# Performance work log

Measured on AMD Instinct MI355X. Metric: run time of the kernel, lower is better.

The kernel has to match this reference:

```python
import jax, jax.numpy as jnp
import numpy as np

N_NODES = 100000
EPS = 1e-07


def _gconv(src, dst, x, W, b):
    # DGL GraphConv with norm='both': D_dst^{-1/2} A (D_src^{-1/2} x) W + b
    ones = jnp.ones(src.shape[0], x.dtype)
    deg_out = jax.ops.segment_sum(ones, src, num_segments=N_NODES)
    deg_in = jax.ops.segment_sum(ones, dst, num_segments=N_NODES)
    norm_out = jnp.where(deg_out > 0, deg_out, 1.0) ** -0.5
    norm_in = jnp.where(deg_in > 0, deg_in, 1.0) ** -0.5
    h = x * norm_out[:, None]
    agg = jax.ops.segment_sum(h[src], dst, num_segments=N_NODES)  # [N, d]
    agg = agg * norm_in[:, None]
    return agg @ W + b


def _branch(npemb, gauss, unif, temp, Wm, bm, Wl, bl, Wq, bq, Wd1, bd1, WdX, bdX, Wc, bc):
    cat = unif.shape[-1]
    mean = npemb @ Wm + bm                      # [E, d_z]
    logstd = npemb @ Wl + bl                    # [E, d_z]
    Nlat = gauss * jnp.exp(logstd) + mean       # reparameterization
    Nlat = Nlat.reshape(npemb.shape[0], cat, -1)  # [E, cat, d_m]
    q = npemb @ Wq + bq                         # [E, cat]
    gumbel = -jnp.log(-jnp.log(unif + EPS) + EPS)
    Z = jax.nn.softmax((q + gumbel) / temp, axis=-1)  # [E, cat]
    M = jnp.einsum('ec,ecd->ed', Z, Nlat)       # [E, d_m]
    X = jax.nn.relu(jax.nn.relu(M @ Wd1 + bd1) @ WdX + bdX)
    A = jax.nn.softmax(M @ Wc + bc, axis=-1)
    return A, X, mean, logstd, q


def setup_inputs() -> dict:
    key = jax.random.key(0)
    ks = jax.random.split(key, 32)
    E_g, E = 800000, 262144
    d_in, d_h, d_z, cat, d_m, d_dec, d_out = 128, 256, 256, 4, 64, 256, 128
    s = 0.05
    inp = {
        'x': jax.random.normal(ks[0], (N_NODES, d_in), jnp.float32),
        'src': jax.random.randint(ks[1], (E_g,), 0, N_NODES),
        'dst': jax.random.randint(ks[2], (E_g,), 0, N_NODES),
        'pos_src': jax.random.randint(ks[3], (E,), 0, N_NODES),
        'pos_dst': jax.random.randint(ks[4], (E,), 0, N_NODES),
        'neg_src': jax.random.randint(ks[5], (E,), 0, N_NODES),
        'neg_dst': jax.random.randint(ks[6], (E,), 0, N_NODES),
        'gauss_pos': jax.random.normal(ks[7], (E, d_z), jnp.float32),
        'gauss_neg': jax.random.normal(ks[8], (E, d_z), jnp.float32),
        'unif_pos': jax.random.uniform(ks[9], (E, cat), jnp.float32),
        'unif_neg': jax.random.uniform(ks[10], (E, cat), jnp.float32),
        'temp': 1,
        'W1': jax.random.normal(ks[11], (d_in, d_h), jnp.float32) * s,
        'b1': jnp.zeros((d_h,), jnp.float32),
        'W2': jax.random.normal(ks[12], (d_h, d_h), jnp.float32) * s,
        'b2': jnp.zeros((d_h,), jnp.float32),
        'Wm': jax.random.normal(ks[13], (d_h, d_z), jnp.float32) * s,
        'bm': jnp.zeros((d_z,), jnp.float32),
        'Wl': jax.random.normal(ks[14], (d_h, d_z), jnp.float32) * s,
        'bl': jnp.zeros((d_z,), jnp.float32),
        'Wq': jax.random.normal(ks[15], (d_h, cat), jnp.float32) * s,
        'bq': jnp.zeros((cat,), jnp.float32),
        'Wd1': jax.random.normal(ks[16], (d_m, d_dec), jnp.float32) * s,
        'bd1': jnp.zeros((d_dec,), jnp.float32),
        'WdX': jax.random.normal(ks[17], (d_dec, d_out), jnp.float32) * s,
        'bdX': jnp.zeros((d_out,), jnp.float32),
        'Wc': jax.random.normal(ks[18], (d_m, cat), jnp.float32) * s,
        'bc': jnp.zeros((cat,), jnp.float32),
    }
    return inp


def reference(x, src, dst, pos_src, pos_dst, neg_src, neg_dst,
              gauss_pos, gauss_neg, unif_pos, unif_neg, temp,
              W1, b1, W2, b2, Wm, bm, Wl, bl, Wq, bq,
              Wd1, bd1, WdX, bdX, Wc, bc):
    # two-layer GraphConv encoder (relu after layer 0; dropout in eval mode = identity)
    h = jax.nn.relu(_gconv(src, dst, x, W1, b1))
    h = _gconv(src, dst, h, W2, b2)
    # u_add_v edge gather
    pos_npemb = h[pos_src] + h[pos_dst]
    neg_npemb = h[neg_src] + h[neg_dst]
    t = jnp.asarray(temp, h.dtype)
    posA, posX, pos_mean, pos_logstd, posq = _branch(
        pos_npemb, gauss_pos, unif_pos, t, Wm, bm, Wl, bl, Wq, bq, Wd1, bd1, WdX, bdX, Wc, bc)
    negA, negX, neg_mean, neg_logstd, negq = _branch(
        neg_npemb, gauss_neg, unif_neg, t, Wm, bm, Wl, bl, Wq, bq, Wd1, bd1, WdX, bdX, Wc, bc)
    return (posA, negA, posX, negX, pos_mean, neg_mean,
            pos_logstd, neg_logstd, posq, negq)
```

## Files before the change

kernel.cpp:

```cpp
#include <hip/hip_runtime.h>
#include <hip/hip_bf16.h>


#define NN 100000
#define EG 800000
#define EE 262144
#define NB 98

typedef __attribute__((ext_vector_type(8))) short short8;
typedef __attribute__((ext_vector_type(4))) float f32x4;

__device__ __forceinline__ float bf2f(unsigned u16) {
  union { unsigned u; float f; } v; v.u = u16 << 16; return v.f;
}
__device__ __forceinline__ float lo2f(unsigned u) {
  union { unsigned u; float f; } v; v.u = u << 16; return v.f;
}
__device__ __forceinline__ float hi2f(unsigned u) {
  union { unsigned u; float f; } v; v.u = u & 0xFFFF0000u; return v.f;
}
__device__ __forceinline__ unsigned short f2bf(float f) {
  union { float f; unsigned u; } v; v.f = f;
  return (unsigned short)((v.u + 0x7FFFu + ((v.u >> 16) & 1u)) >> 16);
}
__device__ __forceinline__ unsigned pack2bf(float a, float b) {
  return (unsigned)f2bf(a) | ((unsigned)f2bf(b) << 16);
}
__device__ __forceinline__ int permc(int c) {
  return (c & ~31) | ((c & 15) << 1) | ((c >> 4) & 1);
}

__device__ __forceinline__ float decode_scalar(const void* p) {
  unsigned u = *(const unsigned*)p;
  float f = __uint_as_float(u);
  float af = fabsf(f);
  if (af >= 1e-6f && af <= 1e6f) return f;
  if (u < 1024u) return (float)u;
  return 1.0f;
}

__global__ __launch_bounds__(256) void k_deg(const int* __restrict__ src,
                                             const int* __restrict__ dst,
                                             int* __restrict__ degO,
                                             int* __restrict__ degI) {
  for (int i = blockIdx.x * 256 + threadIdx.x; i < EG; i += gridDim.x * 256) {
    atomicAdd(&degO[src[i]], 1);
    atomicAdd(&degI[dst[i]], 1);
  }
}

__global__ __launch_bounds__(256) void k_norm(const int* __restrict__ degO,
                                              const int* __restrict__ degI,
                                              float* __restrict__ normO,
                                              float* __restrict__ normI) {
  int i = blockIdx.x * 256 + threadIdx.x;
  if (i < NN) {
    int dO = degO[i]; if (dO < 1) dO = 1;
    int dI = degI[i]; if (dI < 1) dI = 1;
    normO[i] = rsqrtf((float)dO);
    normI[i] = rsqrtf((float)dI);
  }
}

__global__ __launch_bounds__(1024) void k_scan1(const int* __restrict__ degI,
                                                int* __restrict__ rowptr,
                                                int* __restrict__ bsum) {
  __shared__ int wsum[16];
  int t = threadIdx.x, lane = t & 63, wv = t >> 6;
  int i = blockIdx.x * 1024 + t;
  int v = (i < NN) ? degI[i] : 0;
  int incl = v;
#pragma unroll
  for (int off = 1; off < 64; off <<= 1) {
    int u = __shfl_up(incl, off);
    if (lane >= off) incl += u;
  }
  if (lane == 63) wsum[wv] = incl;
  __syncthreads();
  if (wv == 0 && lane < 16) {
    int s = wsum[lane];
    int si = s;
#pragma unroll
    for (int off = 1; off < 16; off <<= 1) {
      int u = __shfl_up(si, off);
      if (lane >= off) si += u;
    }
    wsum[lane] = si - s;
    if (lane == 15) bsum[blockIdx.x] = si;
  }
  __syncthreads();
  int excl = wsum[wv] + incl - v;
  if (i < NN) rowptr[i] = excl;
}

__global__ __launch_bounds__(128) void k_scan2(int* __restrict__ bsum) {
  __shared__ int w0tot;
  int t = threadIdx.x, lane = t & 63, wv = t >> 6;
  int v = (t < NB) ? bsum[t] : 0;
  int incl = v;
#pragma unroll
  for (int off = 1; off < 64; off <<= 1) {
    int u = __shfl_up(incl, off);
    if (lane >= off) incl += u;
  }
  if (wv == 0 && lane == 63) w0tot = incl;
  __syncthreads();
  int excl = incl - v + (wv ? w0tot : 0);
  if (t < NB) bsum[t] = excl;
}

__global__ __launch_bounds__(1024) void k_scan3(const int* __restrict__ degI,
                                                int* __restrict__ rowptr,
                                                int* __restrict__ cursor,
                                                const int* __restrict__ bsum) {
  int i = blockIdx.x * 1024 + threadIdx.x;
  if (i < NN) {
    int vv = rowptr[i] + bsum[blockIdx.x];
    rowptr[i] = vv;
    cursor[i] = vv;
    if (i == NN - 1) rowptr[NN] = vv + degI[i];
  }
}

__global__ __launch_bounds__(256) void k_fill(const int* __restrict__ src,
                                              const int* __restrict__ dst,
                                              int* __restrict__ cursor,
                                              int* __restrict__ csr) {
  for (int e = blockIdx.x * 256 + threadIdx.x; e < EG; e += gridDim.x * 256) {
    int d = dst[e];
    int pos = atomicAdd(&cursor[d], 1);
    csr[pos] = src[e];
  }
}

__global__ __launch_bounds__(256) void k_transpose(const float* __restrict__ in,
                                                   unsigned short* __restrict__ out,
                                                   int K, int Nmask, int logN, int total) {
  for (int idx = blockIdx.x * 256 + threadIdx.x; idx < total; idx += gridDim.x * 256) {
    int n = idx & Nmask;
    int k = idx >> logN;
    out[(size_t)n * K + k] = f2bf(in[idx]);
  }
}

__global__ __launch_bounds__(256) void k_transpose_q(const float* __restrict__ Wq,
                                                     unsigned short* __restrict__ WqT) {
  int idx = blockIdx.x * 256 + threadIdx.x;
  if (idx < 4096) {
    int r = idx >> 8, k = idx & 255;
    WqT[idx] = (r < 4) ? f2bf(Wq[k * 4 + r]) : (unsigned short)0;
  }
}

__global__ __launch_bounds__(256) void k_gather1(
    const float* __restrict__ x, const int* __restrict__ rowptr,
    const int* __restrict__ csr, const float* __restrict__ normO,
    const float* __restrict__ normI, unsigned short* __restrict__ agg) {
  int wid = (blockIdx.x * 256 + threadIdx.x) >> 6;
  int lane = threadIdx.x & 63;
  int half = lane >> 5, fl = lane & 31;
  int nw = (gridDim.x * 256) >> 6;
  for (int n = wid; n < NN; n += nw) {
    int beg = rowptr[n], end = rowptr[n + 1];
    float a0 = 0.f, a1 = 0.f, a2 = 0.f, a3 = 0.f;
    for (int i = beg + half; i < end; i += 2) {
      int s = csr[i];
      float ns = normO[s];
      float4 v = *(const float4*)(x + ((size_t)s << 7) + (fl << 2));
      a0 += ns * v.x; a1 += ns * v.y; a2 += ns * v.z; a3 += ns * v.w;
    }
    a0 += __shfl_xor(a0, 32); a1 += __shfl_xor(a1, 32);
    a2 += __shfl_xor(a2, 32); a3 += __shfl_xor(a3, 32);
    if (lane < 32) {
      float ni = normI[n];
      *(uint2*)(agg + ((size_t)n << 7) + (fl << 2)) =
          make_uint2(pack2bf(a0 * ni, a1 * ni), pack2bf(a2 * ni, a3 * ni));
    }
  }
}

__global__ __launch_bounds__(256) void k_gather2(
    const unsigned short* __restrict__ h1s, const int* __restrict__ rowptr,
    const int* __restrict__ csr, const float* __restrict__ normI,
    unsigned short* __restrict__ agg) {
  int wid = (blockIdx.x * 256 + threadIdx.x) >> 6;
  int lane = threadIdx.x & 63;
  int half = lane >> 5, fl = lane & 31;
  int nw = (gridDim.x * 256) >> 6;
  for (int n = wid; n < NN; n += nw) {
    int beg = rowptr[n], end = rowptr[n + 1];
    float a0 = 0.f, a1 = 0.f, a2 = 0.f, a3 = 0.f, a4 = 0.f, a5 = 0.f, a6 = 0.f, a7 = 0.f;
    for (int i = beg + half; i < end; i += 2) {
      int s = csr[i];
      uint4 v = *(const uint4*)(h1s + ((size_t)s << 8) + (fl << 3));
      a0 += lo2f(v.x); a1 += hi2f(v.x);
      a2 += lo2f(v.y); a3 += hi2f(v.y);
      a4 += lo2f(v.z); a5 += hi2f(v.z);
      a6 += lo2f(v.w); a7 += hi2f(v.w);
    }
    a0 += __shfl_xor(a0, 32); a1 += __shfl_xor(a1, 32);
    a2 += __shfl_xor(a2, 32); a3 += __shfl_xor(a3, 32);
    a4 += __shfl_xor(a4, 32); a5 += __shfl_xor(a5, 32);
    a6 += __shfl_xor(a6, 32); a7 += __shfl_xor(a7, 32);
    if (lane < 32) {
      float ni = normI[n];
      uint4 o;
      o.x = pack2bf(a0 * ni, a1 * ni);
      o.y = pack2bf(a2 * ni, a3 * ni);
      o.z = pack2bf(a4 * ni, a5 * ni);
      o.w = pack2bf(a6 * ni, a7 * ni);
      *(uint4*)(agg + ((size_t)n << 8) + (fl << 3)) = o;
    }
  }
}

template <int K, bool RELU, bool OSCALE>
__global__ __launch_bounds__(256) void k_gemm(
    const unsigned short* __restrict__ A, const float* __restrict__ oscale,
    const unsigned short* __restrict__ WT, const float* __restrict__ bias,
    unsigned short* __restrict__ C, int M) {
  __shared__ __align__(16) short At[128 * 40];
  __shared__ __align__(16) short Bt[256 * 40];
  const int t = threadIdx.x;
  const int row0 = blockIdx.x * 128;
  const int lane = t & 63, wave = t >> 6;
  const int wr = (wave >> 1) << 6;
  const int wcc = (wave & 1) << 7;
  const int lrow = lane & 15, lhi = lane >> 4;

  f32x4 acc[4][8];
#pragma unroll
  for (int m = 0; m < 4; ++m)
#pragma unroll
    for (int n = 0; n < 8; ++n) acc[m][n] = (f32x4){0.f, 0.f, 0.f, 0.f};

  for (int k0 = 0; k0 < K; k0 += 32) {
    if (k0) __syncthreads();
#pragma unroll
    for (int it = 0; it < 2; ++it) {
      int idx = t + it * 256;
      int r = idx >> 2, c8 = (idx & 3) << 3;
      int grow = row0 + r;
      int4 tv = {0, 0, 0, 0};
      if (grow < M) tv = *(const int4*)(A + (size_t)grow * K + k0 + c8);
      *(int4*)&At[r * 40 + c8] = tv;
    }
    {
      const unsigned short* wt = WT + (size_t)permc(t) * K + k0;
      *(int4*)&Bt[t * 40 + 0] = *(const int4*)(wt);
      *(int4*)&Bt[t * 40 + 8] = *(const int4*)(wt + 8);
      *(int4*)&Bt[t * 40 + 16] = *(const int4*)(wt + 16);
      *(int4*)&Bt[t * 40 + 24] = *(const int4*)(wt + 24);
    }
    __syncthreads();
    short8 a[4], b[8];
#pragma unroll
    for (int m = 0; m < 4; ++m)
      a[m] = *(const short8*)&At[(wr + m * 16 + lrow) * 40 + lhi * 8];
#pragma unroll
    for (int n = 0; n < 8; ++n)
      b[n] = *(const short8*)&Bt[(wcc + n * 16 + lrow) * 40 + lhi * 8];
#pragma unroll
    for (int m = 0; m < 4; ++m)
#pragma unroll
      for (int n = 0; n < 8; ++n)
        acc[m][n] = __builtin_amdgcn_mfma_f32_16x16x32_bf16(a[m], b[n], acc[m][n], 0, 0, 0);
  }
#pragma unroll
  for (int np = 0; np < 4; ++np) {
    int tc = wcc + np * 32 + (lrow << 1);
    float bv0 = bias[tc], bv1 = bias[tc + 1];
#pragma unroll
    for (int m = 0; m < 4; ++m) {
#pragma unroll
      for (int r = 0; r < 4; ++r) {
        int grow = row0 + wr + m * 16 + lhi * 4 + r;
        if (grow < M) {
          float v0 = acc[m][2 * np][r] + bv0;
          float v1 = acc[m][2 * np + 1][r] + bv1;
          if (RELU) { v0 = fmaxf(v0, 0.f); v1 = fmaxf(v1, 0.f); }
          if (OSCALE) { float s = oscale[grow]; v0 *= s; v1 *= s; }
          *(unsigned*)&C[(size_t)grow * 256 + tc] = pack2bf(v0, v1);
        }
      }
    }
  }
}

__global__ __launch_bounds__(512) void k_branch2(
    const unsigned short* __restrict__ h, const int* __restrict__ ea,
    const int* __restrict__ eb, const float* __restrict__ gauss,
    const float* __restrict__ unif, const void* __restrict__ temp_p,
    const unsigned short* __restrict__ WmT, const float* __restrict__ bm,
    const unsigned short* __restrict__ WlT, const float* __restrict__ bl,
    const unsigned short* __restrict__ WqT, const float* __restrict__ bq,
    const float* __restrict__ Wc, const float* __restrict__ bc,
    float* __restrict__ o_mean, float* __restrict__ o_ls,
    float* __restrict__ q_o, float* __restrict__ A_o,
    unsigned* __restrict__ M_o32) {
  __shared__ __align__(16) char U[41984];
  short* At = (short*)U;
  short* Btm = (short*)(U + 8192);
  short* Btl = (short*)(U + 24576);
  short* Btq = (short*)(U + 40960);
  float* Mf = (float*)U;
  __shared__ float zS[512];
  __shared__ float WcT[4 * 68];
  __shared__ float bmS[256], blS[256];
  __shared__ int eaS[128], ebS[128];

  const int t = threadIdx.x;
  const int e0 = blockIdx.x << 7;
  const int lane = t & 63;
  const int wv = t >> 6;
  const int lrow = lane & 15, lhi = lane >> 4;
  const int wc = wv << 5;

  if (t < 256) {
    bmS[t] = bm[t]; blS[t] = bl[t];
    WcT[(t & 3) * 68 + (t >> 2)] = Wc[t];
  } else if (t < 384) {
    eaS[t - 256] = ea[e0 + t - 256];
  } else {
    ebS[t - 384] = eb[e0 + t - 384];
  }
  __syncthreads();

  f32x4 am[8][2], al[8][2], aq;
#pragma unroll
  for (int m = 0; m < 8; ++m)
#pragma unroll
    for (int n = 0; n < 2; ++n) {
      am[m][n] = (f32x4){0.f, 0.f, 0.f, 0.f};
      al[m][n] = (f32x4){0.f, 0.f, 0.f, 0.f};
    }
  aq = (f32x4){0.f, 0.f, 0.f, 0.f};

  const int ar = t >> 2, as_ = t & 3;
  const int arsw = ((as_ ^ (ar & 3)) << 3);
  const int br = t & 255, bw = t >> 8;
  const int fsw = (lrow & 3);

  for (int k0 = 0; k0 < 256; k0 += 32) {
    if (k0) __syncthreads();
    {
      const unsigned short* pa = h + ((size_t)eaS[ar] << 8) + k0 + (as_ << 3);
      const unsigned short* pb = h + ((size_t)ebS[ar] << 8) + k0 + (as_ << 3);
      uint4 va = *(const uint4*)pa;
      uint4 vb = *(const uint4*)pb;
      unsigned w0 = pack2bf(lo2f(va.x) + lo2f(vb.x), hi2f(va.x) + hi2f(vb.x));
      unsigned w1 = pack2bf(lo2f(va.y) + lo2f(vb.y), hi2f(va.y) + hi2f(vb.y));
      unsigned w2 = pack2bf(lo2f(va.z) + lo2f(vb.z), hi2f(va.z) + hi2f(vb.z));
      unsigned w3 = pack2bf(lo2f(va.w) + lo2f(vb.w), hi2f(va.w) + hi2f(vb.w));
      *(int4*)&At[ar * 32 + arsw] = make_int4((int)w0, (int)w1, (int)w2, (int)w3);
    }
    {
      const unsigned short* wsrc = (bw ? WlT : WmT) + ((size_t)permc(br) << 8) + k0;
      short* bb = (bw ? Btl : Btm) + br * 32;
      int rs = br & 3;
      *(int4*)&bb[((0 ^ rs) << 3)] = *(const int4*)(wsrc);
      *(int4*)&bb[((1 ^ rs) << 3)] = *(const int4*)(wsrc + 8);
      *(int4*)&bb[((2 ^ rs) << 3)] = *(const int4*)(wsrc + 16);
      *(int4*)&bb[((3 ^ rs) << 3)] = *(const int4*)(wsrc + 24);
    }
    if (t < 64) {
      int r = t >> 2, s = t & 3;
      *(int4*)&Btq[r * 32 + ((s ^ (r & 3)) << 3)] =
          *(const int4*)(WqT + ((size_t)r << 8) + k0 + (s << 3));
    }
    __syncthreads();
    short8 a[8], bmf[2], blf[2], bqf, aqa;
#pragma unroll
    for (int m = 0; m < 8; ++m)
      a[m] = *(const short8*)&At[(m * 16 + lrow) * 32 + ((lhi ^ fsw) << 3)];
#pragma unroll
    for (int n = 0; n < 2; ++n) {
      bmf[n] = *(const short8*)&Btm[(wc + n * 16 + lrow) * 32 + ((lhi ^ fsw) << 3)];
      blf[n] = *(const short8*)&Btl[(wc + n * 16 + lrow) * 32 + ((lhi ^ fsw) << 3)];
    }
    bqf = *(const short8*)&Btq[lrow * 32 + ((lhi ^ fsw) << 3)];
    aqa = *(const short8*)&At[((wv << 4) + lrow) * 32 + ((lhi ^ fsw) << 3)];
#pragma unroll
    for (int m = 0; m < 8; ++m)
#pragma unroll
      for (int n = 0; n < 2; ++n) {
        am[m][n] = __builtin_amdgcn_mfma_f32_16x16x32_bf16(a[m], bmf[n], am[m][n], 0, 0, 0);
        al[m][n] = __builtin_amdgcn_mfma_f32_16x16x32_bf16(a[m], blf[n], al[m][n], 0, 0, 0);
      }
    aq = __builtin_amdgcn_mfma_f32_16x16x32_bf16(aqa, bqf, aq, 0, 0, 0);
  }
  __syncthreads();

  float invt = 1.0f / decode_scalar(temp_p);
  float qb = (lrow < 4) ? bq[lrow] : 0.f;
#pragma unroll
  for (int r = 0; r < 4; ++r) {
    int el = (wv << 4) + lhi * 4 + r;
    float q = aq[r] + qb;
    float uu = 0.5f;
    if (lrow < 4) {
      q_o[(((size_t)(e0 + el)) << 2) + lrow] = q;
      uu = unif[(((size_t)(e0 + el)) << 2) + lrow];
    }
    float g = -__logf(-__logf(uu + 1e-7f) + 1e-7f);
    float z = (q + g) * invt;
    float mx = fmaxf(z, __shfl_xor(z, 1));
    mx = fmaxf(mx, __shfl_xor(mx, 2));
    float ez = __expf(z - mx);
    float sz = ez + __shfl_xor(ez, 1);
    sz += __shfl_xor(sz, 2);
    if (lrow < 4) zS[el * 4 + lrow] = ez / sz;
  }
  for (int i = t; i < 128 * 66; i += 512) Mf[i] = 0.f;
  __syncthreads();

  const int cidx = wv >> 1;
  const int dd = ((wv & 1) << 5) + (lrow << 1);
  const int tc = wc + (lrow << 1);
  float bm0 = bmS[tc], bm1 = bmS[tc + 1];
  float bl0 = blS[tc], bl1 = blS[tc + 1];
#pragma unroll
  for (int m = 0; m < 8; ++m) {
#pragma unroll
    for (int r = 0; r < 4; ++r) {
      int row = m * 16 + lhi * 4 + r;
      size_t gi = (((size_t)(e0 + row)) << 8) + tc;
      float mv0 = am[m][0][r] + bm0, mv1 = am[m][1][r] + bm1;
      float lv0 = al[m][0][r] + bl0, lv1 = al[m][1][r] + bl1;
      *(float2*)(o_mean + gi) = make_float2(mv0, mv1);
      *(float2*)(o_ls + gi) = make_float2(lv0, lv1);
      float2 g2 = *(const float2*)(gauss + gi);
      float zc = zS[(row << 2) + cidx];
      float nl0 = g2.x * __expf(lv0) + mv0;
      float nl1 = g2.y * __expf(lv1) + mv1;
      atomicAdd(&Mf[row * 66 + dd], zc * nl0);
      atomicAdd(&Mf[row * 66 + dd + 1], zc * nl1);
    }
  }
  __syncthreads();

  {
    int e = t >> 2, cat = t & 3;
    const float* mrow = &Mf[e * 66];
    const float* wct = &WcT[cat * 68];
    float s = 0.f;
#pragma unroll
    for (int dp = 0; dp < 32; ++dp) {
      float2 m2 = *(const float2*)(mrow + 2 * dp);
      s += m2.x * wct[2 * dp] + m2.y * wct[2 * dp + 1];
    }
    s += bc[cat];
    float smx = fmaxf(s, __shfl_xor(s, 1));
    smx = fmaxf(smx, __shfl_xor(smx, 2));
    float es = __expf(s - smx);
    float ssum = es + __shfl_xor(es, 1);
    ssum += __shfl_xor(ssum, 2);
    A_o[(((size_t)e0) << 2) + t] = es / ssum;
  }
#pragma unroll
  for (int j = 0; j < 8; ++j) {
    int idx = j * 512 + t;
    int row = idx >> 5, dp = idx & 31;
    float2 m2 = *(const float2*)(&Mf[row * 66 + 2 * dp]);
    M_o32[((size_t)(e0 + row)) * 32 + dp] = pack2bf(m2.x, m2.y);
  }
}

__global__ __launch_bounds__(512) void k_dec2(
    const unsigned short* __restrict__ Mw, const unsigned short* __restrict__ Wd1T,
    const float* __restrict__ bd1, const unsigned short* __restrict__ WdXT,
    const float* __restrict__ bdX, float* __restrict__ Xo) {
  __shared__ __align__(16) char R[65280];
  short* Mt = (short*)R;
  short* Bt1 = (short*)(R + 9216);
  short* X1 = (short*)R;
  short* Bt2 = (short*)(R + 46848);
  const int t = threadIdx.x, lane = t & 63, wv = t >> 6;
  const int lrow = lane & 15, lhi = lane >> 4;
  const int e0 = blockIdx.x << 6;

  {
    int r = t >> 3, c8 = (t & 7) << 3;
    *(int4*)&Mt[r * 72 + c8] = *(const int4*)(Mw + (((size_t)(e0 + r)) << 6) + c8);
  }
  {
    int r1 = t >> 1, base = (t & 1) << 5;
    const unsigned short* wp = Wd1T + ((size_t)permc(r1) << 6) + base;
#pragma unroll
    for (int j = 0; j < 4; ++j)
      *(int4*)&Bt1[r1 * 72 + base + j * 8] = *(const int4*)(wp + j * 8);
  }
  __syncthreads();
  f32x4 acc1[4][2];
#pragma unroll
  for (int m = 0; m < 4; ++m)
#pragma unroll
    for (int n = 0; n < 2; ++n) acc1[m][n] = (f32x4){0.f, 0.f, 0.f, 0.f};
  const int wc1 = wv << 5;
  {
    short8 a0[4], a1[4], b0[2], b1[2];
#pragma unroll
    for (int m = 0; m < 4; ++m) {
      a0[m] = *(const short8*)&Mt[(m * 16 + lrow) * 72 + lhi * 8];
      a1[m] = *(const short8*)&Mt[(m * 16 + lrow) * 72 + 32 + lhi * 8];
    }
#pragma unroll
    for (int n = 0; n < 2; ++n) {
      b0[n] = *(const short8*)&Bt1[(wc1 + n * 16 + lrow) * 72 + lhi * 8];
      b1[n] = *(const short8*)&Bt1[(wc1 + n * 16 + lrow) * 72 + 32 + lhi * 8];
    }
#pragma unroll
    for (int m = 0; m < 4; ++m)
#pragma unroll
      for (int n = 0; n < 2; ++n) {
        acc1[m][n] = __builtin_amdgcn_mfma_f32_16x16x32_bf16(a0[m], b0[n], acc1[m][n], 0, 0, 0);
        acc1[m][n] = __builtin_amdgcn_mfma_f32_16x16x32_bf16(a1[m], b1[n], acc1[m][n], 0, 0, 0);
      }
  }
  __syncthreads();
  {
    int tc = wc1 + (lrow << 1);
    float bdv0 = bd1[tc], bdv1 = bd1[tc + 1];
#pragma unroll
    for (int m = 0; m < 4; ++m)
#pragma unroll
      for (int r = 0; r < 4; ++r) {
        int row = m * 16 + lhi * 4 + r;
        float v0 = fmaxf(acc1[m][0][r] + bdv0, 0.f);
        float v1 = fmaxf(acc1[m][1][r] + bdv1, 0.f);
        *(unsigned*)&X1[row * 264 + tc] = pack2bf(v0, v1);
      }
  }

  f32x4 acc2[2][2];
#pragma unroll
  for (int m = 0; m < 2; ++m)
#pragma unroll
    for (int n = 0; n < 2; ++n) acc2[m][n] = (f32x4){0.f, 0.f, 0.f, 0.f};
  const int wr2 = (wv >> 2) << 5, wc2 = (wv & 3) << 5;
  for (int k0 = 0; k0 < 256; k0 += 64) {
    __syncthreads();
    {
      int r = t >> 2, base = (t & 3) << 4;
      const unsigned short* wp = WdXT + ((size_t)permc(r) << 8) + k0 + base;
      *(int4*)&Bt2[r * 72 + base] = *(const int4*)(wp);
      *(int4*)&Bt2[r * 72 + base + 8] = *(const int4*)(wp + 8);
    }
    __syncthreads();
    short8 c0[2], c1[2], d0[2], d1[2];
#pragma unroll
    for (int m = 0; m < 2; ++m) {
      c0[m] = *(const short8*)&X1[(wr2 + m * 16 + lrow) * 264 + k0 + lhi * 8];
      c1[m] = *(const short8*)&X1[(wr2 + m * 16 + lrow) * 264 + k0 + 32 + lhi * 8];
    }
#pragma unroll
    for (int n = 0; n < 2; ++n) {
      d0[n] = *(const short8*)&Bt2[(wc2 + n * 16 + lrow) * 72 + lhi * 8];
      d1[n] = *(const short8*)&Bt2[(wc2 + n * 16 + lrow) * 72 + 32 + lhi * 8];
    }
#pragma unroll
    for (int m = 0; m < 2; ++m)
#pragma unroll
      for (int n = 0; n < 2; ++n) {
        acc2[m][n] = __builtin_amdgcn_mfma_f32_16x16x32_bf16(c0[m], d0[n], acc2[m][n], 0, 0, 0);
        acc2[m][n] = __builtin_amdgcn_mfma_f32_16x16x32_bf16(c1[m], d1[n], acc2[m][n], 0, 0, 0);
      }
  }
  {
    int tc2 = wc2 + (lrow << 1);
    float bx0 = bdX[tc2], bx1 = bdX[tc2 + 1];
#pragma unroll
    for (int m = 0; m < 2; ++m)
#pragma unroll
      for (int r = 0; r < 4; ++r) {
        int row = wr2 + m * 16 + lhi * 4 + r;
        float v0 = fmaxf(acc2[m][0][r] + bx0, 0.f);
        float v1 = fmaxf(acc2[m][1][r] + bx1, 0.f);
        *(float2*)(Xo + (((size_t)(e0 + row)) << 7) + tc2) = make_float2(v0, v1);
      }
  }
}

extern "C" void kernel_launch(void* const* d_in, const int* in_sizes, int n_in,
                              void* d_out, int out_size, void* d_ws, size_t ws_size,
                              hipStream_t stream) {
  const float* x = (const float*)d_in[0];
  const int* src = (const int*)d_in[1];
  const int* dst = (const int*)d_in[2];
  const int* pos_src = (const int*)d_in[3];
  const int* pos_dst = (const int*)d_in[4];
  const int* neg_src = (const int*)d_in[5];
  const int* neg_dst = (const int*)d_in[6];
  const float* gauss_pos = (const float*)d_in[7];
  const float* gauss_neg = (const float*)d_in[8];
  const float* unif_pos = (const float*)d_in[9];
  const float* unif_neg = (const float*)d_in[10];
  const void* temp_p = d_in[11];
  const float* W1 = (const float*)d_in[12];
  const float* b1 = (const float*)d_in[13];
  const float* W2 = (const float*)d_in[14];
  const float* b2 = (const float*)d_in[15];
  const float* Wm = (const float*)d_in[16];
  const float* bm = (const float*)d_in[17];
  const float* Wl = (const float*)d_in[18];
  const float* bl = (const float*)d_in[19];
  const float* Wq = (const float*)d_in[20];
  const float* bq = (const float*)d_in[21];
  const float* Wd1 = (const float*)d_in[22];
  const float* bd1 = (const float*)d_in[23];
  const float* WdX = (const float*)d_in[24];
  const float* bdX = (const float*)d_in[25];
  const float* Wc = (const float*)d_in[26];
  const float* bc = (const float*)d_in[27];

  char* w = (char*)d_ws;
  int* degO = (int*)w;
  int* degI = (int*)(w + 401408);
  int* rowptr = (int*)(w + 802816);
  int* cursor = (int*)(w + 1204224);
  float* normO = (float*)(w + 1605632);
  float* normI = (float*)(w + 2007040);
  int* csr = (int*)(w + 2408448);
  unsigned short* W1T = (unsigned short*)(w + 5609472);
  unsigned short* W2T = (unsigned short*)(w + 5675008);
  unsigned short* WmT = (unsigned short*)(w + 5806080);
  unsigned short* WlT = (unsigned short*)(w + 5937152);
  unsigned short* Wd1T = (unsigned short*)(w + 6068224);
  unsigned short* WdXT = (unsigned short*)(w + 6100992);
  unsigned short* WqT = (unsigned short*)(w + 6166528);
  int* bsum = (int*)(w + 6174720);
  unsigned short* agg1 = (unsigned short*)(w + 6175232);
  unsigned short* h1s = (unsigned short*)(w + 31775232);
  unsigned short* agg2 = (unsigned short*)(w + 82975232);
  unsigned short* h = (unsigned short*)(w + 134175232);
  unsigned short* Mws = (unsigned short*)(w + 185375232);

  float* out = (float*)d_out;
  float* posA = out;
  float* negA = out + 1048576ull;
  float* posX = out + 2097152ull;
  float* negX = out + 35651584ull;
  float* pos_mean = out + 69206016ull;
  float* neg_mean = out + 136314880ull;
  float* pos_logstd = out + 203423744ull;
  float* neg_logstd = out + 270532608ull;
  float* posq = out + 337641472ull;
  float* negq = out + 338690048ull;

  hipMemsetAsync(d_ws, 0, 802816, stream);

  k_deg<<<1024, 256, 0, stream>>>(src, dst, degO, degI);
  k_norm<<<392, 256, 0, stream>>>(degO, degI, normO, normI);
  k_scan1<<<NB, 1024, 0, stream>>>(degI, rowptr, bsum);
  k_scan2<<<1, 128, 0, stream>>>(bsum);
  k_scan3<<<NB, 1024, 0, stream>>>(degI, rowptr, cursor, bsum);
  k_fill<<<1024, 256, 0, stream>>>(src, dst, cursor, csr);

  k_transpose<<<128, 256, 0, stream>>>(W1, W1T, 128, 255, 8, 32768);
  k_transpose<<<256, 256, 0, stream>>>(W2, W2T, 256, 255, 8, 65536);
  k_transpose<<<256, 256, 0, stream>>>(Wm, WmT, 256, 255, 8, 65536);
  k_transpose<<<256, 256, 0, stream>>>(Wl, WlT, 256, 255, 8, 65536);
  k_transpose<<<64, 256, 0, stream>>>(Wd1, Wd1T, 64, 255, 8, 16384);
  k_transpose<<<128, 256, 0, stream>>>(WdX, WdXT, 256, 127, 7, 32768);
  k_transpose_q<<<16, 256, 0, stream>>>(Wq, WqT);

  k_gather1<<<2048, 256, 0, stream>>>(x, rowptr, csr, normO, normI, agg1);
  k_gemm<128, true, true><<<782, 256, 0, stream>>>(agg1, normO, W1T, b1, h1s, NN);
  k_gather2<<<2048, 256, 0, stream>>>(h1s, rowptr, csr, normI, agg2);
  k_gemm<256, false, false><<<782, 256, 0, stream>>>(agg2, nullptr, W2T, b2, h, NN);

  for (int b = 0; b < 2; ++b) {
    const int* es = b ? neg_src : pos_src;
    const int* ed = b ? neg_dst : pos_dst;
    const float* gs = b ? gauss_neg : gauss_pos;
    const float* uf = b ? unif_neg : unif_pos;
    float* o_mean = b ? neg_mean : pos_mean;
    float* o_ls = b ? neg_logstd : pos_logstd;
    float* o_q = b ? negq : posq;
    float* o_A = b ? negA : posA;
    float* o_X = b ? negX : posX;

    k_branch2<<<2048, 512, 0, stream>>>(h, es, ed, gs, uf, temp_p,
                                        WmT, bm, WlT, bl, WqT, bq, Wc, bc,
                                        o_mean, o_ls, o_q, o_A, (unsigned*)Mws);
    k_dec2<<<4096, 512, 0, stream>>>(Mws, Wd1T, bd1, WdXT, bdX, o_X);
  }
}
```

Baseline: 1.575 ms.

## Fuse small setup kernels, prefetch branch tiles, use nontemporal output stores

Folds the degree-normalisation kernel into the final scan kernel and merges the seven weight-transpose launches into one kernel, cutting launch count. In the branch kernels, the next gathered edge-embedding slice and the next WdX weight slice are loaded into registers one k-step ahead to overlap global loads with MFMA work. The q writes are staged through shared memory so they go out as one coalesced store. Large outputs (mean, logstd, A, X) and the gauss input now use nontemporal stores and loads to reduce cache pollution, at the cost of more register pressure from the prefetch buffers.

```diff
diff --git a/kernel.cpp b/kernel.cpp
--- a/kernel.cpp
+++ b/kernel.cpp
@@ -9,10 +9,8 @@
 
 typedef __attribute__((ext_vector_type(8))) short short8;
 typedef __attribute__((ext_vector_type(4))) float f32x4;
-
-__device__ __forceinline__ float bf2f(unsigned u16) {
-  union { unsigned u; float f; } v; v.u = u16 << 16; return v.f;
-}
+typedef __attribute__((ext_vector_type(2))) float f32x2;
+
 __device__ __forceinline__ float lo2f(unsigned u) {
   union { unsigned u; float f; } v; v.u = u << 16; return v.f;
 }
@@ -46,19 +44,6 @@
   for (int i = blockIdx.x * 256 + threadIdx.x; i < EG; i += gridDim.x * 256) {
     atomicAdd(&degO[src[i]], 1);
     atomicAdd(&degI[dst[i]], 1);
-  }
-}
-
-__global__ __launch_bounds__(256) void k_norm(const int* __restrict__ degO,
-                                              const int* __restrict__ degI,
-                                              float* __restrict__ normO,
-                                              float* __restrict__ normI) {
-  int i = blockIdx.x * 256 + threadIdx.x;
-  if (i < NN) {
-    int dO = degO[i]; if (dO < 1) dO = 1;
-    int dI = degI[i]; if (dI < 1) dI = 1;
-    normO[i] = rsqrtf((float)dO);
-    normI[i] = rsqrtf((float)dI);
   }
 }
 
@@ -110,15 +95,22 @@
 }
 
 __global__ __launch_bounds__(1024) void k_scan3(const int* __restrict__ degI,
+                                                const int* __restrict__ degO,
                                                 int* __restrict__ rowptr,
                                                 int* __restrict__ cursor,
-                                                const int* __restrict__ bsum) {
+                                                const int* __restrict__ bsum,
+                                                float* __restrict__ normO,
+                                                float* __restrict__ normI) {
   int i = blockIdx.x * 1024 + threadIdx.x;
   if (i < NN) {
     int vv = rowptr[i] + bsum[blockIdx.x];
     rowptr[i] = vv;
     cursor[i] = vv;
     if (i == NN - 1) rowptr[NN] = vv + degI[i];
+    int dO = degO[i]; if (dO < 1) dO = 1;
+    int dI = degI[i]; if (dI < 1) dI = 1;
+    normO[i] = rsqrtf((float)dO);
+    normI[i] = rsqrtf((float)dI);
   }
 }
 
@@ -133,22 +125,43 @@
   }
 }
 
-__global__ __launch_bounds__(256) void k_transpose(const float* __restrict__ in,
-                                                   unsigned short* __restrict__ out,
-                                                   int K, int Nmask, int logN, int total) {
-  for (int idx = blockIdx.x * 256 + threadIdx.x; idx < total; idx += gridDim.x * 256) {
-    int n = idx & Nmask;
-    int k = idx >> logN;
-    out[(size_t)n * K + k] = f2bf(in[idx]);
-  }
-}
-
-__global__ __launch_bounds__(256) void k_transpose_q(const float* __restrict__ Wq,
-                                                     unsigned short* __restrict__ WqT) {
+__global__ __launch_bounds__(256) void k_transpose_all(
+    const float* __restrict__ W1, const float* __restrict__ W2,
+    const float* __restrict__ Wm, const float* __restrict__ Wl,
+    const float* __restrict__ Wd1, const float* __restrict__ WdX,
+    const float* __restrict__ Wq,
+    unsigned short* __restrict__ W1T, unsigned short* __restrict__ W2T,
+    unsigned short* __restrict__ WmT, unsigned short* __restrict__ WlT,
+    unsigned short* __restrict__ Wd1T, unsigned short* __restrict__ WdXT,
+    unsigned short* __restrict__ WqT) {
   int idx = blockIdx.x * 256 + threadIdx.x;
-  if (idx < 4096) {
-    int r = idx >> 8, k = idx & 255;
-    WqT[idx] = (r < 4) ? f2bf(Wq[k * 4 + r]) : (unsigned short)0;
+  if (idx < 32768) {
+    int n = idx & 255, k = idx >> 8;
+    W1T[n * 128 + k] = f2bf(W1[idx]);
+  } else if (idx < 98304) {
+    int i = idx - 32768;
+    int n = i & 255, k = i >> 8;
+    W2T[n * 256 + k] = f2bf(W2[i]);
+  } else if (idx < 163840) {
+    int i = idx - 98304;
+    int n = i & 255, k = i >> 8;
+    WmT[n * 256 + k] = f2bf(Wm[i]);
+  } else if (idx < 229376) {
+    int i = idx - 163840;
+    int n = i & 255, k = i >> 8;
+    WlT[n * 256 + k] = f2bf(Wl[i]);
+  } else if (idx < 245760) {
+    int i = idx - 229376;
+    int n = i & 255, k = i >> 8;
+    Wd1T[n * 64 + k] = f2bf(Wd1[i]);
+  } else if (idx < 278528) {
+    int i = idx - 245760;
+    int n = i & 127, k = i >> 7;
+    WdXT[n * 256 + k] = f2bf(WdX[i]);
+  } else if (idx < 282624) {
+    int i = idx - 278528;
+    int r = i >> 8, k = i & 255;
+    WqT[i] = (r < 4) ? f2bf(Wq[k * 4 + r]) : (unsigned short)0;
   }
 }
 
@@ -305,6 +318,7 @@
   short* Btq = (short*)(U + 40960);
   float* Mf = (float*)U;
   __shared__ float zS[512];
+  __shared__ float qS[512];
   __shared__ float WcT[4 * 68];
   __shared__ float bmS[256], blS[256];
   __shared__ int eaS[128], ebS[128];
@@ -341,23 +355,28 @@
   const int br = t & 255, bw = t >> 8;
   const int fsw = (lrow & 3);
 
+  const unsigned short* pa_base = h + ((size_t)eaS[ar] << 8) + (as_ << 3);
+  const unsigned short* pb_base = h + ((size_t)ebS[ar] << 8) + (as_ << 3);
+  const unsigned short* wsrc_base = (bw ? WlT : WmT) + ((size_t)permc(br) << 8);
+  short* bb = (bw ? Btl : Btm) + br * 32;
+  const int rs = br & 3;
+
+  uint4 va = *(const uint4*)pa_base;
+  uint4 vb = *(const uint4*)pb_base;
+
   for (int k0 = 0; k0 < 256; k0 += 32) {
+    unsigned w0 = pack2bf(lo2f(va.x) + lo2f(vb.x), hi2f(va.x) + hi2f(vb.x));
+    unsigned w1 = pack2bf(lo2f(va.y) + lo2f(vb.y), hi2f(va.y) + hi2f(vb.y));
+    unsigned w2 = pack2bf(lo2f(va.z) + lo2f(vb.z), hi2f(va.z) + hi2f(vb.z));
+    unsigned w3 = pack2bf(lo2f(va.w) + lo2f(vb.w), hi2f(va.w) + hi2f(vb.w));
+    if (k0 < 224) {
+      va = *(const uint4*)(pa_base + k0 + 32);
+      vb = *(const uint4*)(pb_base + k0 + 32);
+    }
     if (k0) __syncthreads();
+    *(int4*)&At[ar * 32 + arsw] = make_int4((int)w0, (int)w1, (int)w2, (int)w3);
     {
-      const unsigned short* pa = h + ((size_t)eaS[ar] << 8) + k0 + (as_ << 3);
-      const unsigned short* pb = h + ((size_t)ebS[ar] << 8) + k0 + (as_ << 3);
-      uint4 va = *(const uint4*)pa;
-      uint4 vb = *(const uint4*)pb;
-      unsigned w0 = pack2bf(lo2f(va.x) + lo2f(vb.x), hi2f(va.x) + hi2f(vb.x));
-      unsigned w1 = pack2bf(lo2f(va.y) + lo2f(vb.y), hi2f(va.y) + hi2f(vb.y));
-      unsigned w2 = pack2bf(lo2f(va.z) + lo2f(vb.z), hi2f(va.z) + hi2f(vb.z));
-      unsigned w3 = pack2bf(lo2f(va.w) + lo2f(vb.w), hi2f(va.w) + hi2f(vb.w));
-      *(int4*)&At[ar * 32 + arsw] = make_int4((int)w0, (int)w1, (int)w2, (int)w3);
-    }
-    {
-      const unsigned short* wsrc = (bw ? WlT : WmT) + ((size_t)permc(br) << 8) + k0;
-      short* bb = (bw ? Btl : Btm) + br * 32;
-      int rs = br & 3;
+      const unsigned short* wsrc = wsrc_base + k0;
       *(int4*)&bb[((0 ^ rs) << 3)] = *(const int4*)(wsrc);
       *(int4*)&bb[((1 ^ rs) << 3)] = *(const int4*)(wsrc + 8);
       *(int4*)&bb[((2 ^ rs) << 3)] = *(const int4*)(wsrc + 16);
@@ -398,10 +417,7 @@
     int el = (wv << 4) + lhi * 4 + r;
     float q = aq[r] + qb;
     float uu = 0.5f;
-    if (lrow < 4) {
-      q_o[(((size_t)(e0 + el)) << 2) + lrow] = q;
-      uu = unif[(((size_t)(e0 + el)) << 2) + lrow];
-    }
+    if (lrow < 4) uu = unif[(((size_t)(e0 + el)) << 2) + lrow];
     float g = -__logf(-__logf(uu + 1e-7f) + 1e-7f);
     float z = (q + g) * invt;
     float mx = fmaxf(z, __shfl_xor(z, 1));
@@ -409,10 +425,12 @@
     float ez = __expf(z - mx);
     float sz = ez + __shfl_xor(ez, 1);
     sz += __shfl_xor(sz, 2);
-    if (lrow < 4) zS[el * 4 + lrow] = ez / sz;
+    if (lrow < 4) { zS[el * 4 + lrow] = ez / sz; qS[el * 4 + lrow] = q; }
   }
   for (int i = t; i < 128 * 66; i += 512) Mf[i] = 0.f;
   __syncthreads();
+
+  __builtin_nontemporal_store(qS[t], q_o + (((size_t)e0) << 2) + t);
 
   const int cidx = wv >> 1;
   const int dd = ((wv & 1) << 5) + (lrow << 1);
@@ -427,14 +445,12 @@
       size_t gi = (((size_t)(e0 + row)) << 8) + tc;
       float mv0 = am[m][0][r] + bm0, mv1 = am[m][1][r] + bm1;
       float lv0 = al[m][0][r] + bl0, lv1 = al[m][1][r] + bl1;
-      *(float2*)(o_mean + gi) = make_float2(mv0, mv1);
-      *(float2*)(o_ls + gi) = make_float2(lv0, lv1);
-      float2 g2 = *(const float2*)(gauss + gi);
+      __builtin_nontemporal_store((f32x2){mv0, mv1}, (f32x2*)(o_mean + gi));
+      __builtin_nontemporal_store((f32x2){lv0, lv1}, (f32x2*)(o_ls + gi));
+      f32x2 g2 = __builtin_nontemporal_load((const f32x2*)(gauss + gi));
       float zc = zS[(row << 2) + cidx];
-      float nl0 = g2.x * __expf(lv0) + mv0;
-      float nl1 = g2.y * __expf(lv1) + mv1;
-      atomicAdd(&Mf[row * 66 + dd], zc * nl0);
-      atomicAdd(&Mf[row * 66 + dd + 1], zc * nl1);
+      atomicAdd(&Mf[row * 66 + dd], zc * (g2.x * __expf(lv0) + mv0));
+      atomicAdd(&Mf[row * 66 + dd + 1], zc * (g2.y * __expf(lv1) + mv1));
     }
   }
   __syncthreads();
@@ -455,7 +471,7 @@
     float es = __expf(s - smx);
     float ssum = es + __shfl_xor(es, 1);
     ssum += __shfl_xor(ssum, 2);
-    A_o[(((size_t)e0) << 2) + t] = es / ssum;
+    __builtin_nontemporal_store(es / ssum, A_o + (((size_t)e0) << 2) + t);
   }
 #pragma unroll
   for (int j = 0; j < 8; ++j) {
@@ -479,6 +495,9 @@
   const int lrow = lane & 15, lhi = lane >> 4;
   const int e0 = blockIdx.x << 6;
 
+  const int r2 = t >> 2, base2 = (t & 3) << 4;
+  const unsigned short* wpb = WdXT + ((size_t)permc(r2) << 8) + base2;
+
   {
     int r = t >> 3, c8 = (t & 7) << 3;
     *(int4*)&Mt[r * 72 + c8] = *(const int4*)(Mw + (((size_t)(e0 + r)) << 6) + c8);
@@ -490,6 +509,8 @@
     for (int j = 0; j < 4; ++j)
       *(int4*)&Bt1[r1 * 72 + base + j * 8] = *(const int4*)(wp + j * 8);
   }
+  int4 pw0 = *(const int4*)(wpb);
+  int4 pw1 = *(const int4*)(wpb + 8);
   __syncthreads();
   f32x4 acc1[4][2];
 #pragma unroll
@@ -540,11 +561,11 @@
   const int wr2 = (wv >> 2) << 5, wc2 = (wv & 3) << 5;
   for (int k0 = 0; k0 < 256; k0 += 64) {
     __syncthreads();
-    {
-      int r = t >> 2, base = (t & 3) << 4;
-      const unsigned short* wp = WdXT + ((size_t)permc(r) << 8) + k0 + base;
-      *(int4*)&Bt2[r * 72 + base] = *(const int4*)(wp);
-      *(int4*)&Bt2[r * 72 + base + 8] = *(const int4*)(wp + 8);
+    *(int4*)&Bt2[r2 * 72 + base2] = pw0;
+    *(int4*)&Bt2[r2 * 72 + base2 + 8] = pw1;
+    if (k0 < 192) {
+      pw0 = *(const int4*)(wpb + k0 + 64);
+      pw1 = *(const int4*)(wpb + k0 + 64 + 8);
     }
     __syncthreads();
     short8 c0[2], c1[2], d0[2], d1[2];
@@ -576,7 +597,8 @@
         int row = wr2 + m * 16 + lhi * 4 + r;
         float v0 = fmaxf(acc2[m][0][r] + bx0, 0.f);
         float v1 = fmaxf(acc2[m][1][r] + bx1, 0.f);
-        *(float2*)(Xo + (((size_t)(e0 + row)) << 7) + tc2) = make_float2(v0, v1);
+        __builtin_nontemporal_store((f32x2){v0, v1},
+                                    (f32x2*)(Xo + (((size_t)(e0 + row)) << 7) + tc2));
       }
   }
 }
@@ -650,19 +672,12 @@
   hipMemsetAsync(d_ws, 0, 802816, stream);
 
   k_deg<<<1024, 256, 0, stream>>>(src, dst, degO, degI);
-  k_norm<<<392, 256, 0, stream>>>(degO, degI, normO, normI);
   k_scan1<<<NB, 1024, 0, stream>>>(degI, rowptr, bsum);
   k_scan2<<<1, 128, 0, stream>>>(bsum);
-  k_scan3<<<NB, 1024, 0, stream>>>(degI, rowptr, cursor, bsum);
+  k_scan3<<<NB, 1024, 0, stream>>>(degI, degO, rowptr, cursor, bsum, normO, normI);
   k_fill<<<1024, 256, 0, stream>>>(src, dst, cursor, csr);
-
-  k_transpose<<<128, 256, 0, stream>>>(W1, W1T, 128, 255, 8, 32768);
-  k_transpose<<<256, 256, 0, stream>>>(W2, W2T, 256, 255, 8, 65536);
-  k_transpose<<<256, 256, 0, stream>>>(Wm, WmT, 256, 255, 8, 65536);
-  k_transpose<<<256, 256, 0, stream>>>(Wl, WlT, 256, 255, 8, 65536);
-  k_transpose<<<64, 256, 0, stream>>>(Wd1, Wd1T, 64, 255, 8, 16384);
-  k_transpose<<<128, 256, 0, stream>>>(WdX, WdXT, 256, 127, 7, 32768);
-  k_transpose_q<<<16, 256, 0, stream>>>(Wq, WqT);
+  k_transpose_all<<<1104, 256, 0, stream>>>(W1, W2, Wm, Wl, Wd1, WdX, Wq,
+                                            W1T, W2T, WmT, WlT, Wd1T, WdXT, WqT);
 
   k_gather1<<<2048, 256, 0, stream>>>(x, rowptr, csr, normO, normI, agg1);
   k_gemm<128, true, true><<<782, 256, 0, stream>>>(agg1, normO, W1T, b1, h1s, NN);
```

Result: faster. 1.491 ms (-5.3%).
